# Kernel tuning notes

Hardware: AMD Instinct MI355X
Metric: run time of the kernel (lower is better)

Reference implementation:

```python
import jax, jax.numpy as jnp
import numpy as np

# --- model constants (reconstructed LIF + exponential-PSP semantics) ---
V_TH = 1.0        # spike threshold
V_DECAY = 0.9     # membrane leak per ms
PSP_DECAY = 0.8   # postsynaptic-potential filter decay
BETA = 5.0        # surrogate-gradient sharpness
D = 16            # spike_buffer depth (max synaptic delay)
H = W = 64
T = 200
N = H * W
N_DEL = 11        # number of delayed synapses


def setup_inputs() -> dict:
    key = jax.random.key(0)
    ks = jax.random.split(key, 5)
    stim = jax.random.uniform(ks[0], (H, W, T), dtype=jnp.float32) * 8.0
    scale = 1.0 / np.sqrt(N)
    W_sa_in = jax.random.normal(ks[1], (N, N), dtype=jnp.float32) * scale
    W_ra_in = jax.random.normal(ks[2], (N, N), dtype=jnp.float32) * scale
    W_del = jax.random.normal(ks[3], (N_DEL, N, N), dtype=jnp.float32) * scale
    delays = jax.random.randint(ks[4], (N_DEL, N), 0, D, dtype=jnp.int32)
    return {"stim": stim, "W_sa_in": W_sa_in, "W_ra_in": W_ra_in,
            "W_del": W_del, "delays": delays}


def _spike(v):
    """Hard threshold forward, sigmoid surrogate gradient (straight-through)."""
    hard = (v >= V_TH).astype(v.dtype)
    soft = jax.nn.sigmoid(BETA * (v - V_TH))
    return soft + jax.lax.stop_gradient(hard - soft)


def reference(stim, W_sa_in, W_ra_in, W_del, delays):
    n = stim.shape[0] * stim.shape[1]
    t_len = stim.shape[2]
    # stimulus preprocessing (feedforward):
    sa_stim = (stim - 3.0).reshape(n, t_len)                    # [N, T]
    d = jnp.abs(jnp.diff(stim, axis=2)) * 10.0                  # [H, W, T-1]
    d = d.at[:, :, :3].set(0.0)
    ra_stim = jnp.concatenate(
        [jnp.zeros(stim.shape[:2] + (1,), stim.dtype), d], axis=2
    ).reshape(n, t_len)                                         # [N, T]

    idx = jnp.arange(n)
    read_col = D - 1 - delays                                   # [11, N] constant gather columns

    def lif(v, buf, li, inp):
        vn = v[li] * V_DECAY + inp
        s = _spike(vn)
        vn = vn * (1.0 - s)                                     # reset on spike
        v = v.at[li].set(vn)
        buf = buf.at[li].set(
            jnp.concatenate([buf[li][:, 1:], s[:, None]], axis=1))  # roll, newest last
        return v, buf, s

    def syn(psp, k, buf_pre):
        dsp = buf_pre[idx, read_col[k]]                         # per-pre delayed spikes [N]
        p = psp[k] * PSP_DECAY + W_del[k] @ dsp
        return psp.at[k].set(p), p

    def step(carry, xs):
        v, buf, psp = carry
        sa_x, ra_x = xs
        # SA pathway (layers 0,1,2 <-> state rows 0,1,2)
        v, buf, s0 = lif(v, buf, 0, W_sa_in @ sa_x)
        psp, i1 = syn(psp, 0, buf[0])
        v, buf, s1 = lif(v, buf, 1, i1)
        psp, pn1 = syn(psp, 1, buf[0])
        psp, pn2 = syn(psp, 2, buf[1])
        v, buf, s2 = lif(v, buf, 2, 2.0 * pn1 - pn2)
        # RA pathway (state rows 3,4,5)
        v, buf, s3 = lif(v, buf, 3, W_ra_in @ ra_x)
        psp, j1 = syn(psp, 3, buf[3])
        v, buf, s4 = lif(v, buf, 4, j1)
        psp, qn1 = syn(psp, 4, buf[3])
        psp, qn2 = syn(psp, 5, buf[4])
        v, buf, s5 = lif(v, buf, 5, 2.0 * qn1 - qn2)
        # CN (state rows 6 = IN, 7 = PN)
        psp, cin_sa = syn(psp, 6, buf[2])
        psp, cin_ra = syn(psp, 8, buf[5])
        v, buf, s6 = lif(v, buf, 6, cin_sa + cin_ra)
        psp, cpn_sa = syn(psp, 7, buf[2])
        psp, cpn_ra = syn(psp, 9, buf[5])
        psp, inh = syn(psp, 10, buf[6])
        v, buf, s7 = lif(v, buf, 7, 2.0 * cpn_sa + 2.0 * cpn_ra - inh)
        return (v, buf, psp), jnp.stack([s0, s1, s2, s3, s4, s5, s6, s7])

    carry0 = (jnp.zeros((8, n), stim.dtype),
              jnp.zeros((8, n, D), stim.dtype),
              jnp.zeros((N_DEL, n), stim.dtype))
    xs = (sa_stim[:, 1:].T, ra_stim[:, 1:].T)                   # [T-1, N] each
    _, spikes = jax.lax.scan(step, carry0, xs)                  # [T-1, 8, N]
    return jnp.transpose(spikes, (1, 2, 0))                     # [8, N, T-1]
```

## Files before the change

kernel.cpp:

```cpp
#include <hip/hip_runtime.h>

#define NN   4096
#define TLEN 200
#define NT   199
#define NW   8
#define NTP  256
#define TN   ((size_t)NT * NN)
#define TN2  ((size_t)NN * NTP)

#define BM 128
#define BT 128
#define BK 32
#define BMP 132
#define BTP 132

typedef __attribute__((ext_vector_type(8))) short short8;
typedef __attribute__((ext_vector_type(16))) float f32x16;


__global__ __launch_bounds__(256, 2) void gsyn(const float* __restrict__ Wdel,
    const int* __restrict__ delays, const unsigned* __restrict__ Sb,
    float* __restrict__ u, int Slog, int kpack, int prepack, int slotpack) {
  const int z = blockIdx.y;
  const int ki = z >> Slog, s = z & ((1 << Slog) - 1);
  const int k = (kpack >> (4 * ki)) & 15;
  const int pre = (prepack >> (4 * ki)) & 15;
  const int slot = ((slotpack >> (6 * ki)) & 63) + s;
  const int NJ = NN >> Slog;
  const int jbase = s * NJ;
  const float* __restrict__ Wk = Wdel + (size_t)k * NN * NN;
  const unsigned* __restrict__ Sp = Sb + (size_t)pre * NW * NN;
  const int* __restrict__ dl = delays + (size_t)k * NN;
  float* __restrict__ uo = u + (size_t)slot * TN2;

  __shared__ __align__(16) unsigned char smem[3 * 8192 + 16384];
  #define XOFF 24576

  const int i0 = blockIdx.x * 128;
  const int tid = threadIdx.x;
  const int wave = tid >> 6, lane = tid & 63;
  const int m = lane & 31, hb = lane >> 5;
  const int wi = wave >> 1, wt = wave & 1;
  const int bmax = wt ? 3 : 4;

  f32x16 acc[2][4];
  #pragma unroll
  for (int a = 0; a < 2; ++a)
    #pragma unroll
    for (int b = 0; b < 4; ++b) acc[a][b] = 0.0f;

  const int rb = tid >> 3, kc = tid & 7;
  const int kx = tid & 31, tg = tid >> 5;

  for (int j0 = 0; j0 < NJ; j0 += 32) {
    #pragma unroll
    for (int mm = 0; mm < 4; ++mm) {
      const int r = rb + 32 * mm;
      const float4 w4 = *(const float4*)&Wk[(size_t)(i0 + r) * NN + jbase + j0 + kc * 4];
      unsigned h[4], md[4], lo[4];
      const float wv[4] = {w4.x, w4.y, w4.z, w4.w};
      #pragma unroll
      for (int e = 0; e < 4; ++e) {
        const unsigned ub = __float_as_uint(wv[e]);
        h[e] = ub >> 16;
        const float r1 = wv[e] - __uint_as_float(ub & 0xFFFF0000u);
        const unsigned u1 = __float_as_uint(r1);
        md[e] = u1 >> 16;
        const float r2 = r1 - __uint_as_float(u1 & 0xFFFF0000u);
        lo[e] = __float_as_uint(r2) >> 16;
      }
      const unsigned base = (unsigned)((r * 64 + kc * 8) ^ ((r & 7) << 4));
      uint2 p0; p0.x = (h[1] << 16) | h[0];  p0.y = (h[3] << 16) | h[2];
      uint2 p1; p1.x = (md[1] << 16) | md[0]; p1.y = (md[3] << 16) | md[2];
      uint2 p2; p2.x = (lo[1] << 16) | lo[0]; p2.y = (lo[3] << 16) | lo[2];
      *(uint2*)(smem + base)          = p0;
      *(uint2*)(smem + 8192 + base)   = p1;
      *(uint2*)(smem + 16384 + base)  = p2;
    }
    {
      const int j = jbase + j0 + kx;
      const int d = dl[j];
      const int tsrc = tg * 32 - d;
      const int w0 = tsrc >> 5;
      const int sh = tsrc & 31;
      const unsigned blo = (w0 >= 0) ? Sp[(size_t)w0 * NN + j] : 0u;
      const unsigned bhi = (w0 + 1 < NW) ? Sp[(size_t)(w0 + 1) * NN + j] : 0u;
      const unsigned wnd = sh ? ((blo >> sh) | (bhi << (32 - sh))) : blo;
      #pragma unroll
      for (int b = 0; b < 32; ++b) {
        const unsigned short xv = ((wnd >> b) & 1u) ? (unsigned short)0x3F80 : (unsigned short)0;
        const int t = tg * 32 + b;
        *(unsigned short*)(smem + XOFF + ((t * 64 + kx * 2) ^ ((t & 7) << 4))) = xv;
      }
    }
    __syncthreads();
    #pragma unroll
    for (int h2 = 0; h2 < 2; ++h2) {
      const int cb = h2 * 32 + hb * 16;
      short8 bfr[4];
      #pragma unroll
      for (int b = 0; b < 4; ++b) {
        if (b < bmax) {
          const int tr = wt * 128 + b * 32 + m;
          bfr[b] = *(const short8*)(smem + XOFF + ((tr * 64 + cb) ^ ((tr & 7) << 4)));
        }
      }
      #pragma unroll
      for (int a = 0; a < 2; ++a) {
        const int ra = wi * 64 + a * 32 + m;
        const unsigned abase = (unsigned)((ra * 64 + cb) ^ ((ra & 7) << 4));
        const short8 a0 = *(const short8*)(smem + abase);
        const short8 a1 = *(const short8*)(smem + 8192 + abase);
        const short8 a2 = *(const short8*)(smem + 16384 + abase);
        #pragma unroll
        for (int b = 0; b < 4; ++b) {
          if (b < bmax) {
            acc[a][b] = __builtin_amdgcn_mfma_f32_32x32x16_bf16(a0, bfr[b], acc[a][b], 0, 0, 0);
            acc[a][b] = __builtin_amdgcn_mfma_f32_32x32x16_bf16(a1, bfr[b], acc[a][b], 0, 0, 0);
            acc[a][b] = __builtin_amdgcn_mfma_f32_32x32x16_bf16(a2, bfr[b], acc[a][b], 0, 0, 0);
          }
        }
      }
    }
    __syncthreads();
  }
  #pragma unroll
  for (int a = 0; a < 2; ++a)
    #pragma unroll
    for (int b = 0; b < 4; ++b) {
      if (b < bmax) {
        const int tt2 = wt * 128 + b * 32 + m;
        #pragma unroll
        for (int r = 0; r < 16; ++r) {
          const int ii = i0 + wi * 64 + a * 32 + (r & 3) + 8 * (r >> 2) + 4 * hb;
          uo[(size_t)ii * NTP + tt2] = acc[a][b][r];
        }
      }
    }
  #undef XOFF
}

__global__ __launch_bounds__(256, 2) void gstim(const float* __restrict__ Wsa,
    const float* __restrict__ Wra, const float* __restrict__ stim,
    float* __restrict__ u) {
  const int zi = blockIdx.z;
  const int mode = zi >> 2, s = zi & 3;
  const int slot = 64 + 4 * mode + s;
  const int NJ = NN >> 2;
  const int jbase = s * NJ;
  const float* __restrict__ W = mode ? Wra : Wsa;
  float* __restrict__ uo = u + (size_t)slot * TN2;

  __shared__ float Ws[BK][BMP];
  __shared__ float Xs[BK][BTP];
  const int i0 = blockIdx.x * BM;
  const int t0 = blockIdx.y * BT;
  const int tid = threadIdx.x;
  const int rg = tid >> 4, cg = tid & 15;
  float acc[8][8] = {};

  for (int k0 = 0; k0 < NJ; k0 += BK) {
    {
      const int kk4 = tid & 7, r = tid >> 3;
      const int sw = 4 * kk4;
      #pragma unroll
      for (int mq = 0; mq < 4; ++mq) {
        const int rr = r + 32 * mq;
        const float4 w = *(const float4*)&W[(size_t)(i0 + rr) * NN + jbase + k0 + 4 * kk4];
        const int pc = rr ^ sw;
        Ws[4 * kk4 + 0][pc] = w.x; Ws[4 * kk4 + 1][pc] = w.y;
        Ws[4 * kk4 + 2][pc] = w.z; Ws[4 * kk4 + 3][pc] = w.w;
      }
    }
    {
      const int kk = tid >> 3, sb8 = tid & 7;
      const int j = jbase + k0 + kk;
      #pragma unroll
      for (int q = 0; q < 4; ++q) {
        float4 xv;
        float* xp = (float*)&xv;
        #pragma unroll
        for (int e = 0; e < 4; ++e) {
          const int tt = t0 + 16 * sb8 + 4 * q + e;
          float x = 0.0f;
          if (tt < NT) {
            const int tc = tt + 1;
            if (mode == 0) {
              x = stim[(size_t)j * TLEN + tc] - 3.0f;
            } else {
              x = (tc >= 4)
                ? fabsf(stim[(size_t)j * TLEN + tc] - stim[(size_t)j * TLEN + tc - 1]) * 10.0f
                : 0.0f;
            }
          }
          xp[e] = x;
        }
        *(float4*)&Xs[kk][16 * sb8 + 4 * q] = xv;
      }
    }
    __syncthreads();
    #pragma unroll
    for (int kk = 0; kk < BK; ++kk) {
      const int wsw = 4 * (kk >> 2);
      const float4 ra = *(const float4*)&Ws[kk][(rg * 4) ^ wsw];
      const float4 rbv = *(const float4*)&Ws[kk][(64 + rg * 4) ^ wsw];
      const float4 ca = *(const float4*)&Xs[kk][cg * 4];
      const float4 cb = *(const float4*)&Xs[kk][64 + cg * 4];
      const float rv[8] = {ra.x, ra.y, ra.z, ra.w, rbv.x, rbv.y, rbv.z, rbv.w};
      const float cv[8] = {ca.x, ca.y, ca.z, ca.w, cb.x, cb.y, cb.z, cb.w};
      #pragma unroll
      for (int a = 0; a < 8; ++a)
        #pragma unroll
        for (int b = 0; b < 8; ++b) acc[a][b] += rv[a] * cv[b];
    }
    __syncthreads();
  }
  #pragma unroll
  for (int a = 0; a < 8; ++a) {
    const int ia = i0 + ((a < 4) ? (rg * 4 + a) : (64 + rg * 4 + (a - 4)));
    #pragma unroll
    for (int bh = 0; bh < 2; ++bh) {
      float4 o;
      o.x = acc[a][bh * 4 + 0]; o.y = acc[a][bh * 4 + 1];
      o.z = acc[a][bh * 4 + 2]; o.w = acc[a][bh * 4 + 3];
      *(float4*)&uo[(size_t)ia * NTP + t0 + bh * 64 + cg * 4] = o;
    }
  }
}

template<int S>
__device__ __forceinline__ float4 sumS4(const float* __restrict__ u, int slot, int tg, int j) {
  float4 r = {0.f, 0.f, 0.f, 0.f};
  #pragma unroll
  for (int q = 0; q < S; ++q) {
    const float4 a = *(const float4*)&u[(size_t)(slot + q) * TN2 + (size_t)j * NTP + tg];
    r.x += a.x; r.y += a.y; r.z += a.z; r.w += a.w;
  }
  return r;
}
__device__ __forceinline__ float fidx(const float4& v, int q) {
  return q == 0 ? v.x : q == 1 ? v.y : q == 2 ? v.z : v.w;
}

__device__ __forceinline__ void flush_bits(unsigned* sb, int j, int t, unsigned& bits) {
  if ((t & 31) == 31 || t == NT - 1) { sb[(size_t)(t >> 5) * NN + j] = bits; bits = 0; }
}

__global__ void scan_a(const float* __restrict__ u, unsigned* __restrict__ Sb) {
  const int j = blockIdx.x * 64 + threadIdx.x;
  const int base = 64 + 4 * blockIdx.y;
  unsigned* sb = Sb + (size_t)(blockIdx.y ? 3 : 0) * NW * NN;
  float v = 0.f; unsigned bits = 0;
  for (int tg = 0; tg < NT; tg += 4) {
    const float4 in4 = sumS4<4>(u, base, tg, j);
    #pragma unroll
    for (int q = 0; q < 4; ++q) {
      const int t = tg + q;
      if (t < NT) {
        float vn = v * 0.9f + fidx(in4, q);
        unsigned s = vn >= 1.0f;
        v = s ? 0.f : vn;
        bits |= s << (t & 31);
        flush_bits(sb, j, t, bits);
      }
    }
  }
}

__global__ void scan_b(const float* __restrict__ u, unsigned* __restrict__ Sb,
                       float* __restrict__ p1s, float* __restrict__ p4s) {
  const int j = blockIdx.x * 64 + threadIdx.x;
  const int sa = blockIdx.y;
  const int baseA = sa ? 8 : 0, baseB = sa ? 12 : 4;
  float* ps = sa ? p4s : p1s;
  unsigned* sb = Sb + (size_t)(sa ? 4 : 1) * NW * NN;
  float v = 0.f, pa = 0.f, pb = 0.f; unsigned bits = 0;
  for (int tg = 0; tg < NT; tg += 4) {
    const float4 A4 = sumS4<4>(u, baseA, tg, j);
    const float4 B4 = sumS4<4>(u, baseB, tg, j);
    #pragma unroll
    for (int q = 0; q < 4; ++q) {
      const int t = tg + q;
      if (t < NT) {
        pa = pa * 0.8f + fidx(A4, q);
        float vn = v * 0.9f + pa;
        unsigned s = vn >= 1.0f;
        v = s ? 0.f : vn;
        bits |= s << (t & 31);
        flush_bits(sb, j, t, bits);
        pb = pb * 0.8f + fidx(B4, q);
        ps[(size_t)t * NN + j] = 2.0f * pb;
      }
    }
  }
}

__global__ void scan_c(const float* __restrict__ u, unsigned* __restrict__ Sb,
                       const float* __restrict__ p1s, const float* __restrict__ p4s) {
  const int j = blockIdx.x * 64 + threadIdx.x;
  const int sa = blockIdx.y;
  const int base = sa ? 24 : 16;
  const float* ps = sa ? p4s : p1s;
  unsigned* sb = Sb + (size_t)(sa ? 5 : 2) * NW * NN;
  float v = 0.f, p = 0.f; unsigned bits = 0;
  for (int tg = 0; tg < NT; tg += 4) {
    const float4 A4 = sumS4<8>(u, base, tg, j);
    float P[4];
    #pragma unroll
    for (int q = 0; q < 4; ++q)
      P[q] = (tg + q < NT) ? ps[(size_t)(tg + q) * NN + j] : 0.0f;
    #pragma unroll
    for (int q = 0; q < 4; ++q) {
      const int t = tg + q;
      if (t < NT) {
        p = p * 0.8f + fidx(A4, q);
        float vn = v * 0.9f + (P[q] - p);
        unsigned s = vn >= 1.0f;
        v = s ? 0.f : vn;
        bits |= s << (t & 31);
        flush_bits(sb, j, t, bits);
      }
    }
  }
}

__global__ void scan_d(const float* __restrict__ u, unsigned* __restrict__ Sb,
                       float* __restrict__ p79s) {
  const int j = blockIdx.x * 64 + threadIdx.x;
  if (blockIdx.y == 0) {
    unsigned* sb = Sb + (size_t)6 * NW * NN;
    float v = 0.f, p6 = 0.f, p8 = 0.f; unsigned bits = 0;
    for (int tg = 0; tg < NT; tg += 4) {
      const float4 A4 = sumS4<4>(u, 32, tg, j);
      const float4 B4 = sumS4<4>(u, 40, tg, j);
      #pragma unroll
      for (int q = 0; q < 4; ++q) {
        const int t = tg + q;
        if (t < NT) {
          p6 = p6 * 0.8f + fidx(A4, q);
          p8 = p8 * 0.8f + fidx(B4, q);
          float vn = v * 0.9f + (p6 + p8);
          unsigned s = vn >= 1.0f;
          v = s ? 0.f : vn;
          bits |= s << (t & 31);
          flush_bits(sb, j, t, bits);
        }
      }
    }
  } else {
    float p7 = 0.f, p9 = 0.f;
    for (int tg = 0; tg < NT; tg += 4) {
      const float4 A4 = sumS4<4>(u, 36, tg, j);
      const float4 B4 = sumS4<4>(u, 44, tg, j);
      #pragma unroll
      for (int q = 0; q < 4; ++q) {
        const int t = tg + q;
        if (t < NT) {
          p7 = p7 * 0.8f + fidx(A4, q);
          p9 = p9 * 0.8f + fidx(B4, q);
          p79s[(size_t)t * NN + j] = 2.0f * p7 + 2.0f * p9;
        }
      }
    }
  }
}

__global__ void scan_e(const float* __restrict__ u, unsigned* __restrict__ Sb,
                       const float* __restrict__ p79s) {
  const int j = blockIdx.x * 64 + threadIdx.x;
  unsigned* sb = Sb + (size_t)7 * NW * NN;
  float v = 0.f, p = 0.f; unsigned bits = 0;
  for (int tg = 0; tg < NT; tg += 4) {
    const float4 A4 = sumS4<16>(u, 48, tg, j);
    float P[4];
    #pragma unroll
    for (int q = 0; q < 4; ++q)
      P[q] = (tg + q < NT) ? p79s[(size_t)(tg + q) * NN + j] : 0.0f;
    #pragma unroll
    for (int q = 0; q < 4; ++q) {
      const int t = tg + q;
      if (t < NT) {
        p = p * 0.8f + fidx(A4, q);
        float vn = v * 0.9f + (P[q] - p);
        unsigned s = vn >= 1.0f;
        v = s ? 0.f : vn;
        bits |= s << (t & 31);
        flush_bits(sb, j, t, bits);
      }
    }
  }
}

__global__ void expand_k(const unsigned* __restrict__ Sb, float* __restrict__ out) {
  const int j = blockIdx.x * 256 + threadIdx.x;
  const int w = blockIdx.y, li = blockIdx.z;
  unsigned bits = Sb[((size_t)li * NW + w) * NN + j];
  float* o = out + ((size_t)li * NN + j) * NT + w * 32;
  int nb = NT - w * 32; if (nb > 32) nb = 32;
  for (int b = 0; b < nb; ++b) o[b] = (float)((bits >> b) & 1u);
}

extern "C" void kernel_launch(void* const* d_in, const int* in_sizes, int n_in,
                              void* d_out, int out_size, void* d_ws, size_t ws_size,
                              hipStream_t stream) {
  const float* stim   = (const float*)d_in[0];
  const float* Wsa    = (const float*)d_in[1];
  const float* Wra    = (const float*)d_in[2];
  const float* Wdel   = (const float*)d_in[3];
  const int*   delays = (const int*)d_in[4];
  float* out = (float*)d_out;
  float* ws  = (float*)d_ws;

  float* u    = ws;
  float* p1s  = u + 72 * TN2;
  float* p4s  = p1s + TN;
  float* p79s = p4s + TN;
  unsigned* Sb = (unsigned*)(p79s + TN);
  size_t need = (72 * TN2 + 3 * TN + (size_t)8 * NW * NN) * 4;
  if (ws_size < need) return;

  hipMemsetAsync(Sb, 0, (size_t)8 * NW * NN * sizeof(unsigned), stream);

  const dim3 gmf(NN / 128, 16);
  gstim<<<dim3(NN / BM, 2, 8), 256, 0, stream>>>(Wsa, Wra, stim, u);
  scan_a<<<dim3(64, 2), 64, 0, stream>>>(u, Sb);

  gsyn<<<gmf, 256, 0, stream>>>(Wdel, delays, Sb, u, 2, 0x4310, 0x3300,
                                0 | (4 << 6) | (8 << 12) | (12 << 18));
  scan_b<<<dim3(64, 2), 64, 0, stream>>>(u, Sb, p1s, p4s);

  gsyn<<<gmf, 256, 0, stream>>>(Wdel, delays, Sb, u, 3, 0x52, 0x41, 16 | (24 << 6));
  scan_c<<<dim3(64, 2), 64, 0, stream>>>(u, Sb, p1s, p4s);

  gsyn<<<gmf, 256, 0, stream>>>(Wdel, delays, Sb, u, 2, 0x9876, 0x5522,
                                32 | (36 << 6) | (40 << 12) | (44 << 18));
  scan_d<<<dim3(64, 2), 64, 0, stream>>>(u, Sb, p79s);

  gsyn<<<gmf, 256, 0, stream>>>(Wdel, delays, Sb, u, 4, 10, 6, 48);
  scan_e<<<dim3(64, 1), 64, 0, stream>>>(u, Sb, p79s);

  expand_k<<<dim3(16, 7, 8), 256, 0, stream>>>(Sb, out);
}
```

Baseline: 799.9 us.

## Fuse all GEMM and scan stages into one cooperative persistent kernel

Turns the GEMM and scan kernels into device functions and runs them in sequence inside one cooperative kernel of 512 blocks, with grid.sync between stages. If the cooperative launch fails, it falls back to the separate launches. This removes nine kernel launch boundaries and spreads each scan over 512 blocks of 16 threads instead of 64-thread blocks. The cost is that the scan phases leave most threads idle, and all 512 blocks must be resident at once under the 2-blocks-per-CU bound.

```diff
diff --git a/kernel.cpp b/kernel.cpp
--- a/kernel.cpp
+++ b/kernel.cpp
@@ -1,4 +1,6 @@
 #include <hip/hip_runtime.h>
+#include <hip/hip_cooperative_groups.h>
+namespace cg = cooperative_groups;
 
 #define NN   4096
 #define TLEN 200
@@ -14,14 +16,18 @@
 #define BMP 132
 #define BTP 132
 
+#define SLOTPK_A (0 | (4 << 6) | (8 << 12) | (12 << 18))
+#define SLOTPK_C (32 | (36 << 6) | (40 << 12) | (44 << 18))
+
 typedef __attribute__((ext_vector_type(8))) short short8;
 typedef __attribute__((ext_vector_type(16))) float f32x16;
 
 
-__global__ __launch_bounds__(256, 2) void gsyn(const float* __restrict__ Wdel,
+__device__ void gsyn_body(unsigned char* smem, const float* __restrict__ Wdel,
     const int* __restrict__ delays, const unsigned* __restrict__ Sb,
-    float* __restrict__ u, int Slog, int kpack, int prepack, int slotpack) {
-  const int z = blockIdx.y;
+    float* __restrict__ u, int x, int z, int tid,
+    int Slog, int kpack, int prepack, int slotpack) {
+  const int XOFF = 24576;
   const int ki = z >> Slog, s = z & ((1 << Slog) - 1);
   const int k = (kpack >> (4 * ki)) & 15;
   const int pre = (prepack >> (4 * ki)) & 15;
@@ -33,11 +39,7 @@
   const int* __restrict__ dl = delays + (size_t)k * NN;
   float* __restrict__ uo = u + (size_t)slot * TN2;
 
-  __shared__ __align__(16) unsigned char smem[3 * 8192 + 16384];
-  #define XOFF 24576
-
-  const int i0 = blockIdx.x * 128;
-  const int tid = threadIdx.x;
+  const int i0 = x * 128;
   const int wave = tid >> 6, lane = tid & 63;
   const int m = lane & 31, hb = lane >> 5;
   const int wi = wave >> 1, wt = wave & 1;
@@ -137,13 +139,13 @@
         }
       }
     }
-  #undef XOFF
-}
-
-__global__ __launch_bounds__(256, 2) void gstim(const float* __restrict__ Wsa,
+}
+
+__device__ void gstim_body(unsigned char* smem, const float* __restrict__ Wsa,
     const float* __restrict__ Wra, const float* __restrict__ stim,
-    float* __restrict__ u) {
-  const int zi = blockIdx.z;
+    float* __restrict__ u, int bx, int by, int zi, int tid) {
+  float* Ws = (float*)smem;
+  float* Xs = (float*)(smem + 16896);
   const int mode = zi >> 2, s = zi & 3;
   const int slot = 64 + 4 * mode + s;
   const int NJ = NN >> 2;
@@ -151,11 +153,8 @@
   const float* __restrict__ W = mode ? Wra : Wsa;
   float* __restrict__ uo = u + (size_t)slot * TN2;
 
-  __shared__ float Ws[BK][BMP];
-  __shared__ float Xs[BK][BTP];
-  const int i0 = blockIdx.x * BM;
-  const int t0 = blockIdx.y * BT;
-  const int tid = threadIdx.x;
+  const int i0 = bx * BM;
+  const int t0 = by * BT;
   const int rg = tid >> 4, cg = tid & 15;
   float acc[8][8] = {};
 
@@ -168,8 +167,8 @@
         const int rr = r + 32 * mq;
         const float4 w = *(const float4*)&W[(size_t)(i0 + rr) * NN + jbase + k0 + 4 * kk4];
         const int pc = rr ^ sw;
-        Ws[4 * kk4 + 0][pc] = w.x; Ws[4 * kk4 + 1][pc] = w.y;
-        Ws[4 * kk4 + 2][pc] = w.z; Ws[4 * kk4 + 3][pc] = w.w;
+        Ws[(4 * kk4 + 0) * BMP + pc] = w.x; Ws[(4 * kk4 + 1) * BMP + pc] = w.y;
+        Ws[(4 * kk4 + 2) * BMP + pc] = w.z; Ws[(4 * kk4 + 3) * BMP + pc] = w.w;
       }
     }
     {
@@ -195,17 +194,17 @@
           }
           xp[e] = x;
         }
-        *(float4*)&Xs[kk][16 * sb8 + 4 * q] = xv;
+        *(float4*)&Xs[kk * BTP + 16 * sb8 + 4 * q] = xv;
       }
     }
     __syncthreads();
     #pragma unroll
     for (int kk = 0; kk < BK; ++kk) {
       const int wsw = 4 * (kk >> 2);
-      const float4 ra = *(const float4*)&Ws[kk][(rg * 4) ^ wsw];
-      const float4 rbv = *(const float4*)&Ws[kk][(64 + rg * 4) ^ wsw];
-      const float4 ca = *(const float4*)&Xs[kk][cg * 4];
-      const float4 cb = *(const float4*)&Xs[kk][64 + cg * 4];
+      const float4 ra = *(const float4*)&Ws[kk * BMP + ((rg * 4) ^ wsw)];
+      const float4 rbv = *(const float4*)&Ws[kk * BMP + ((64 + rg * 4) ^ wsw)];
+      const float4 ca = *(const float4*)&Xs[kk * BTP + cg * 4];
+      const float4 cb = *(const float4*)&Xs[kk * BTP + 64 + cg * 4];
       const float rv[8] = {ra.x, ra.y, ra.z, ra.w, rbv.x, rbv.y, rbv.z, rbv.w};
       const float cv[8] = {ca.x, ca.y, ca.z, ca.w, cb.x, cb.y, cb.z, cb.w};
       #pragma unroll
@@ -241,15 +240,14 @@
 __device__ __forceinline__ float fidx(const float4& v, int q) {
   return q == 0 ? v.x : q == 1 ? v.y : q == 2 ? v.z : v.w;
 }
-
 __device__ __forceinline__ void flush_bits(unsigned* sb, int j, int t, unsigned& bits) {
   if ((t & 31) == 31 || t == NT - 1) { sb[(size_t)(t >> 5) * NN + j] = bits; bits = 0; }
 }
 
-__global__ void scan_a(const float* __restrict__ u, unsigned* __restrict__ Sb) {
-  const int j = blockIdx.x * 64 + threadIdx.x;
-  const int base = 64 + 4 * blockIdx.y;
-  unsigned* sb = Sb + (size_t)(blockIdx.y ? 3 : 0) * NW * NN;
+__device__ void scan_a_body(const float* __restrict__ u, unsigned* __restrict__ Sb,
+                            int y, int j) {
+  const int base = 64 + 4 * y;
+  unsigned* sb = Sb + (size_t)(y ? 3 : 0) * NW * NN;
   float v = 0.f; unsigned bits = 0;
   for (int tg = 0; tg < NT; tg += 4) {
     const float4 in4 = sumS4<4>(u, base, tg, j);
@@ -267,10 +265,9 @@
   }
 }
 
-__global__ void scan_b(const float* __restrict__ u, unsigned* __restrict__ Sb,
-                       float* __restrict__ p1s, float* __restrict__ p4s) {
-  const int j = blockIdx.x * 64 + threadIdx.x;
-  const int sa = blockIdx.y;
+__device__ void scan_b_body(const float* __restrict__ u, unsigned* __restrict__ Sb,
+                            float* __restrict__ p1s, float* __restrict__ p4s,
+                            int sa, int j) {
   const int baseA = sa ? 8 : 0, baseB = sa ? 12 : 4;
   float* ps = sa ? p4s : p1s;
   unsigned* sb = Sb + (size_t)(sa ? 4 : 1) * NW * NN;
@@ -295,10 +292,9 @@
   }
 }
 
-__global__ void scan_c(const float* __restrict__ u, unsigned* __restrict__ Sb,
-                       const float* __restrict__ p1s, const float* __restrict__ p4s) {
-  const int j = blockIdx.x * 64 + threadIdx.x;
-  const int sa = blockIdx.y;
+__device__ void scan_c_body(const float* __restrict__ u, unsigned* __restrict__ Sb,
+                            const float* __restrict__ p1s, const float* __restrict__ p4s,
+                            int sa, int j) {
   const int base = sa ? 24 : 16;
   const float* ps = sa ? p4s : p1s;
   unsigned* sb = Sb + (size_t)(sa ? 5 : 2) * NW * NN;
@@ -324,10 +320,9 @@
   }
 }
 
-__global__ void scan_d(const float* __restrict__ u, unsigned* __restrict__ Sb,
-                       float* __restrict__ p79s) {
-  const int j = blockIdx.x * 64 + threadIdx.x;
-  if (blockIdx.y == 0) {
+__device__ void scan_d_body(const float* __restrict__ u, unsigned* __restrict__ Sb,
+                            float* __restrict__ p79s, int y, int j) {
+  if (y == 0) {
     unsigned* sb = Sb + (size_t)6 * NW * NN;
     float v = 0.f, p6 = 0.f, p8 = 0.f; unsigned bits = 0;
     for (int tg = 0; tg < NT; tg += 4) {
@@ -365,9 +360,8 @@
   }
 }
 
-__global__ void scan_e(const float* __restrict__ u, unsigned* __restrict__ Sb,
-                       const float* __restrict__ p79s) {
-  const int j = blockIdx.x * 64 + threadIdx.x;
+__device__ void scan_e_body(const float* __restrict__ u, unsigned* __restrict__ Sb,
+                            const float* __restrict__ p79s, int j) {
   unsigned* sb = Sb + (size_t)7 * NW * NN;
   float v = 0.f, p = 0.f; unsigned bits = 0;
   for (int tg = 0; tg < NT; tg += 4) {
@@ -389,6 +383,73 @@
       }
     }
   }
+}
+
+__global__ __launch_bounds__(256, 2) void mega(
+    const float* __restrict__ Wdel, const int* __restrict__ delays,
+    unsigned* __restrict__ Sb, float* __restrict__ u,
+    const float* __restrict__ Wsa, const float* __restrict__ Wra,
+    const float* __restrict__ stim, float* __restrict__ p1s,
+    float* __restrict__ p4s, float* __restrict__ p79s) {
+  cg::grid_group grid = cg::this_grid();
+  __shared__ __align__(16) unsigned char smem[40960];
+  const int bid = blockIdx.x, tid = threadIdx.x;
+  const int gx = bid & 31, gz = bid >> 5;
+
+  gstim_body(smem, Wsa, Wra, stim, u, bid & 31, (bid >> 5) & 1, bid >> 6, tid);
+  grid.sync();
+  if (tid < 16) { const int jj = bid * 16 + tid; scan_a_body(u, Sb, jj >> 12, jj & 4095); }
+  grid.sync();
+  gsyn_body(smem, Wdel, delays, Sb, u, gx, gz, tid, 2, 0x4310, 0x3300, SLOTPK_A);
+  grid.sync();
+  if (tid < 16) { const int jj = bid * 16 + tid; scan_b_body(u, Sb, p1s, p4s, jj >> 12, jj & 4095); }
+  grid.sync();
+  gsyn_body(smem, Wdel, delays, Sb, u, gx, gz, tid, 3, 0x52, 0x41, 16 | (24 << 6));
+  grid.sync();
+  if (tid < 16) { const int jj = bid * 16 + tid; scan_c_body(u, Sb, p1s, p4s, jj >> 12, jj & 4095); }
+  grid.sync();
+  gsyn_body(smem, Wdel, delays, Sb, u, gx, gz, tid, 2, 0x9876, 0x5522, SLOTPK_C);
+  grid.sync();
+  if (tid < 16) { const int jj = bid * 16 + tid; scan_d_body(u, Sb, p79s, jj >> 12, jj & 4095); }
+  grid.sync();
+  gsyn_body(smem, Wdel, delays, Sb, u, gx, gz, tid, 4, 10, 6, 48);
+  grid.sync();
+  if (tid < 8) { const int jj = bid * 8 + tid; scan_e_body(u, Sb, p79s, jj); }
+}
+
+__global__ __launch_bounds__(256, 2) void gsyn_k(const float* __restrict__ Wdel,
+    const int* __restrict__ delays, const unsigned* __restrict__ Sb,
+    float* __restrict__ u, int Slog, int kpack, int prepack, int slotpack) {
+  __shared__ __align__(16) unsigned char smem[40960];
+  gsyn_body(smem, Wdel, delays, Sb, u, blockIdx.x, blockIdx.y, threadIdx.x,
+            Slog, kpack, prepack, slotpack);
+}
+
+__global__ __launch_bounds__(256, 2) void gstim_k(const float* __restrict__ Wsa,
+    const float* __restrict__ Wra, const float* __restrict__ stim,
+    float* __restrict__ u) {
+  __shared__ __align__(16) unsigned char smem[40960];
+  gstim_body(smem, Wsa, Wra, stim, u, blockIdx.x, blockIdx.y, blockIdx.z, threadIdx.x);
+}
+
+__global__ void scan_a_k(const float* __restrict__ u, unsigned* __restrict__ Sb) {
+  scan_a_body(u, Sb, blockIdx.y, blockIdx.x * 64 + threadIdx.x);
+}
+__global__ void scan_b_k(const float* __restrict__ u, unsigned* __restrict__ Sb,
+                         float* __restrict__ p1s, float* __restrict__ p4s) {
+  scan_b_body(u, Sb, p1s, p4s, blockIdx.y, blockIdx.x * 64 + threadIdx.x);
+}
+__global__ void scan_c_k(const float* __restrict__ u, unsigned* __restrict__ Sb,
+                         const float* __restrict__ p1s, const float* __restrict__ p4s) {
+  scan_c_body(u, Sb, p1s, p4s, blockIdx.y, blockIdx.x * 64 + threadIdx.x);
+}
+__global__ void scan_d_k(const float* __restrict__ u, unsigned* __restrict__ Sb,
+                         float* __restrict__ p79s) {
+  scan_d_body(u, Sb, p79s, blockIdx.y, blockIdx.x * 64 + threadIdx.x);
+}
+__global__ void scan_e_k(const float* __restrict__ u, unsigned* __restrict__ Sb,
+                         const float* __restrict__ p79s) {
+  scan_e_body(u, Sb, p79s, blockIdx.x * 64 + threadIdx.x);
 }
 
 __global__ void expand_k(const unsigned* __restrict__ Sb, float* __restrict__ out) {
@@ -421,23 +482,29 @@
 
   hipMemsetAsync(Sb, 0, (size_t)8 * NW * NN * sizeof(unsigned), stream);
 
+  void* params[10];
+  params[0] = (void*)&Wdel;  params[1] = (void*)&delays; params[2] = (void*)&Sb;
+  params[3] = (void*)&u;     params[4] = (void*)&Wsa;    params[5] = (void*)&Wra;
+  params[6] = (void*)&stim;  params[7] = (void*)&p1s;    params[8] = (void*)&p4s;
+  params[9] = (void*)&p79s;
+  hipError_t cerr = hipLaunchCooperativeKernel((const void*)mega, dim3(512), dim3(256),
+                                               params, 0, stream);
+  if (cerr == hipSuccess) {
+    expand_k<<<dim3(16, 7, 8), 256, 0, stream>>>(Sb, out);
+    return;
+  }
+  (void)hipGetLastError();
+
   const dim3 gmf(NN / 128, 16);
-  gstim<<<dim3(NN / BM, 2, 8), 256, 0, stream>>>(Wsa, Wra, stim, u);
-  scan_a<<<dim3(64, 2), 64, 0, stream>>>(u, Sb);
-
-  gsyn<<<gmf, 256, 0, stream>>>(Wdel, delays, Sb, u, 2, 0x4310, 0x3300,
-                                0 | (4 << 6) | (8 << 12) | (12 << 18));
-  scan_b<<<dim3(64, 2), 64, 0, stream>>>(u, Sb, p1s, p4s);
-
-  gsyn<<<gmf, 256, 0, stream>>>(Wdel, delays, Sb, u, 3, 0x52, 0x41, 16 | (24 << 6));
-  scan_c<<<dim3(64, 2), 64, 0, stream>>>(u, Sb, p1s, p4s);
-
-  gsyn<<<gmf, 256, 0, stream>>>(Wdel, delays, Sb, u, 2, 0x9876, 0x5522,
-                                32 | (36 << 6) | (40 << 12) | (44 << 18));
-  scan_d<<<dim3(64, 2), 64, 0, stream>>>(u, Sb, p79s);
-
-  gsyn<<<gmf, 256, 0, stream>>>(Wdel, delays, Sb, u, 4, 10, 6, 48);
-  scan_e<<<dim3(64, 1), 64, 0, stream>>>(u, Sb, p79s);
-
+  gstim_k<<<dim3(NN / BM, 2, 8), 256, 0, stream>>>(Wsa, Wra, stim, u);
+  scan_a_k<<<dim3(64, 2), 64, 0, stream>>>(u, Sb);
+  gsyn_k<<<gmf, 256, 0, stream>>>(Wdel, delays, Sb, u, 2, 0x4310, 0x3300, SLOTPK_A);
+  scan_b_k<<<dim3(64, 2), 64, 0, stream>>>(u, Sb, p1s, p4s);
+  gsyn_k<<<gmf, 256, 0, stream>>>(Wdel, delays, Sb, u, 3, 0x52, 0x41, 16 | (24 << 6));
+  scan_c_k<<<dim3(64, 2), 64, 0, stream>>>(u, Sb, p1s, p4s);
+  gsyn_k<<<gmf, 256, 0, stream>>>(Wdel, delays, Sb, u, 2, 0x9876, 0x5522, SLOTPK_C);
+  scan_d_k<<<dim3(64, 2), 64, 0, stream>>>(u, Sb, p79s);
+  gsyn_k<<<gmf, 256, 0, stream>>>(Wdel, delays, Sb, u, 4, 10, 6, 48);
+  scan_e_k<<<dim3(64, 1), 64, 0, stream>>>(u, Sb, p79s);
   expand_k<<<dim3(16, 7, 8), 256, 0, stream>>>(Sb, out);
 }
```

Result: slower. 2.096 ms (+162.1%).
